# Performance work log

Measured on AMD Instinct MI355X. Metric: run time of the kernel, lower is better.

Reference implementation:

```python
import jax, jax.numpy as jnp
import numpy as np

B, D, K = 32, 400, 200
H = 8            # kernel_size (GRU hidden)
LAYERS = 4
OUT = 8


def setup_inputs() -> dict:
    key = jax.random.key(0)
    ks = jax.random.split(key, 16)
    x = jax.random.normal(ks[0], (B, D, K), dtype=jnp.float32)
    # variable-length zero padding along time per (b, k) sequence
    lengths = jax.random.randint(ks[1], (B, K), D // 2, D + 1)
    tmask = jnp.arange(D)[None, :, None] < lengths[:, None, :]   # (B, D, K)
    x = x * tmask
    s = 1.0 / np.sqrt(H)
    def u(k, shape):
        return jax.random.uniform(k, shape, jnp.float32, -s, s)
    return {
        "x": x,
        "w_ih0": u(ks[2], (2, 3 * H, 1)),
        "w_hh0": u(ks[3], (2, 3 * H, H)),
        "b_ih0": u(ks[4], (2, 3 * H)),
        "b_hh0": u(ks[5], (2, 3 * H)),
        "w_ih": u(ks[6], (LAYERS - 1, 2, 3 * H, 2 * H)),
        "w_hh": u(ks[7], (LAYERS - 1, 2, 3 * H, H)),
        "b_ih": u(ks[8], (LAYERS - 1, 2, 3 * H)),
        "b_hh": u(ks[9], (LAYERS - 1, 2, 3 * H)),
        "lin1_w": u(ks[10], (H, 2 * H)),
        "lin1_b": u(ks[11], (H,)),
        "lin2_w": u(ks[12], (OUT, H)),
        "lin2_b": u(ks[13], (OUT,)),
    }


def _gru_dir(x, mask, Wih, Whh, bih, bhh):
    # x: (N, T, in), mask: (N, T) bool -> (N, T, H); zero past each length
    gi = jnp.einsum('nti,gi->tng', x, Wih) + bih          # (T, N, 3H) input gates
    m = mask.T[:, :, None]                                 # (T, N, 1)
    h0 = jnp.zeros((x.shape[0], Whh.shape[1]), x.dtype)
    def step(h, inp):
        gi_t, m_t = inp
        gh = h @ Whh.T + bhh
        ir, iz, inn = jnp.split(gi_t, 3, axis=-1)          # PyTorch gate order r, z, n
        hr, hz, hn = jnp.split(gh, 3, axis=-1)
        r = jax.nn.sigmoid(ir + hr)
        z = jax.nn.sigmoid(iz + hz)
        n = jnp.tanh(inn + r * hn)
        h = jnp.where(m_t, (1.0 - z) * n + z * h, h)
        return h, jnp.where(m_t, h, 0.0)
    _, out = jax.lax.scan(step, h0, (gi, m))
    return out.transpose(1, 0, 2)


def _bidir_gru(x, mask, rev_idx, p):
    Wih, Whh, bih, bhh = p
    fwd = _gru_dir(x, mask, Wih[0], Whh[0], bih[0], bhh[0])
    # backward dir of a packed sequence: reverse within each valid region
    x_rev = jnp.take_along_axis(x, rev_idx[:, :, None], axis=1)
    bwd_rev = _gru_dir(x_rev, mask, Wih[1], Whh[1], bih[1], bhh[1])
    bwd = jnp.take_along_axis(bwd_rev, rev_idx[:, :, None], axis=1)
    bwd = jnp.where(mask[:, :, None], bwd, 0.0)
    return jnp.concatenate([fwd, bwd], axis=-1)


def _forward(x, w_ih0, w_hh0, b_ih0, b_hh0, w_ih, w_hh, b_ih, b_hh,
             lin1_w, lin1_b, lin2_w, lin2_b):
    b, d, k = x.shape
    seq = x.transpose(0, 2, 1).reshape(b * k, d, 1)         # (N, T, 1)
    vals = seq[:, :, 0]
    zm = vals == 0.0
    lengths = jnp.where(zm.any(axis=1), jnp.argmax(zm, axis=1), d)  # (N,)
    mask = jnp.arange(d)[None, :] < lengths[:, None]        # (N, T)
    rev_idx = jnp.clip(lengths[:, None] - 1 - jnp.arange(d)[None, :], 0, d - 1)
    h = _bidir_gru(seq, mask, rev_idx, (w_ih0, w_hh0, b_ih0, b_hh0))
    for l in range(w_ih.shape[0]):                          # layers 1..3
        h = _bidir_gru(h, mask, rev_idx, (w_ih[l], w_hh[l], b_ih[l], b_hh[l]))
    # last valid timestep per sequence (matches argmax-of-all-zero gather)
    last = jnp.take_along_axis(h, (lengths - 1)[:, None, None], axis=1)[:, 0, :]
    feat = last.reshape(b, k, -1)                           # (B, K, 2H)
    y = jax.nn.leaky_relu(feat @ lin1_w.T + lin1_b, negative_slope=0.2)
    return y @ lin2_w.T + lin2_b                            # (B, K, OUT)


def reference(x, w_ih0, w_hh0, b_ih0, b_hh0, w_ih, w_hh, b_ih, b_hh,
              lin1_w, lin1_b, lin2_w, lin2_b):
    return _forward(x, w_ih0, w_hh0, b_ih0, b_hh0, w_ih, w_hh, b_ih, b_hh,
                    lin1_w, lin1_b, lin2_w, lin2_b)
```

## Files before the change

kernel.cpp:

```cpp
#include <hip/hip_runtime.h>

#define BB 32
#define DD 400
#define KK 200
#define NN (BB*KK)
#define NBINS 512

typedef float f2 __attribute__((ext_vector_type(2)));
typedef _Float16 half_t;
typedef _Float16 f16x2 __attribute__((ext_vector_type(2)));

#if defined(__has_builtin)
#if __has_builtin(__builtin_amdgcn_fdot2)
#define HAVE_FDOT2 1
#endif
#endif

__device__ __forceinline__ float dot2(f16x2 w, f16x2 v, float acc) {
#ifdef HAVE_FDOT2
  return __builtin_amdgcn_fdot2(w, v, acc, false);
#else
  return fmaf((float)w.x, (float)v.x, fmaf((float)w.y, (float)v.y, acc));
#endif
}

__device__ __forceinline__ float fast_sigmoid(float x) {
  float e = __builtin_amdgcn_exp2f(-1.4426950408889634f * x);
  return __builtin_amdgcn_rcpf(1.0f + e);
}
__device__ __forceinline__ float fast_tanh(float x) {
  float e = __builtin_amdgcn_exp2f(-2.8853900817779268f * x);
  return 2.0f * __builtin_amdgcn_rcpf(1.0f + e) - 1.0f;
}

#define QPERM(v, P) __int_as_float(__builtin_amdgcn_mov_dpp(__float_as_int(v), (P)*0x55, 0xF, 0xF, true))
#define HMIRROR(v) __int_as_float(__builtin_amdgcn_mov_dpp(__float_as_int(v), 0x141, 0xF, 0xF, true))

__global__ __launch_bounds__(256) void transpose_x(const float* __restrict__ x,
                                                   float* __restrict__ xt) {
  __shared__ float tile[32][33];
  int b = blockIdx.x, t0 = blockIdx.y * 32, k0 = blockIdx.z * 32;
  int tx = threadIdx.x, ty = threadIdx.y;
#pragma unroll
  for (int i = 0; i < 32; i += 8) {
    int t = t0 + ty + i, k = k0 + tx;
    tile[ty + i][tx] = (t < DD && k < KK) ? x[((size_t)b * DD + t) * KK + k] : 0.0f;
  }
  __syncthreads();
#pragma unroll
  for (int i = 0; i < 32; i += 8) {
    int k = k0 + ty + i, t = t0 + tx;
    if (k < KK && t < DD) xt[((size_t)b * KK + k) * DD + t] = tile[tx][ty + i];
  }
}

__global__ __launch_bounds__(64) void compute_lengths(const float* __restrict__ xt,
                                                      int* __restrict__ lengths,
                                                      int* __restrict__ hist) {
  int n = blockIdx.x, lane = threadIdx.x;
  int m = DD;
  for (int t = lane; t < DD; t += 64) {
    if (xt[(size_t)n * DD + t] == 0.0f) { m = t; break; }
  }
#pragma unroll
  for (int off = 1; off < 64; off <<= 1) {
    int o = __shfl_xor(m, off, 64);
    m = (o < m) ? o : m;
  }
  if (lane == 0) {
    lengths[n] = m;
    atomicAdd(&hist[m], 1);
  }
}

__global__ __launch_bounds__(64) void scan_offsets(const int* __restrict__ hist,
                                                   int* __restrict__ offs) {
  int lane = threadIdx.x;
  int v[8], tot = 0;
#pragma unroll
  for (int i = 0; i < 8; ++i) { v[i] = tot; tot += hist[lane * 8 + i]; }
  int incl = tot;
#pragma unroll
  for (int off = 1; off < 64; off <<= 1) {
    int oth = __shfl_up(incl, off, 64);
    if (lane >= off) incl += oth;
  }
  int excl = incl - tot;
#pragma unroll
  for (int i = 0; i < 8; ++i) offs[lane * 8 + i] = excl + v[i];
}

__global__ __launch_bounds__(256) void scatter_sort(const int* __restrict__ lengths,
                                                    int* __restrict__ offs,
                                                    int* __restrict__ order,
                                                    int* __restrict__ len_sorted) {
  int n = blockIdx.x * 256 + threadIdx.x;
  if (n >= NN) return;
  int len = lengths[n];
  int pos = atomicAdd(&offs[len], 1);
  order[pos] = n;
  len_sorted[pos] = len;
}

template <int IN_DIM, bool IND_IN, bool WRITE_SEQ, bool FWD_ONLY>
__global__ __launch_bounds__(256) void gru_scan(
    const void* __restrict__ in, half_t* __restrict__ out, float* __restrict__ feat,
    const int* __restrict__ len_sorted, const int* __restrict__ order,
    const float* __restrict__ Wih, const float* __restrict__ Whh,
    const float* __restrict__ bih, const float* __restrict__ bhh, int nseq) {
  int p = (blockIdx.x * 256 + threadIdx.x) >> 6;
  int lane = threadIdx.x & 63;
  int G = FWD_ONLY ? nseq : nseq * 2;
  int W = (G + 7) >> 3;
  if (p >= W) return;
  int o = (p & 1) ? (W - 1 - (p >> 1)) : (p >> 1);
  int gidx = o * 8 + (lane >> 3);
  int li = lane & 7;
  if (gidx >= G) return;
  int sg  = FWD_ONLY ? gidx : (gidx >> 1);
  int dir = FWD_ONLY ? 0 : (gidx & 1);
  int len = len_sorted[sg];

  int qb = li & 4;
  f2 wAB[3][4];
  f16x2 wi2[3][8];
  float wi1[3];
  float bs[3], bh2;
#pragma unroll
  for (int gt = 0; gt < 3; ++gt) {
    int row = dir * 24 + gt * 8 + li;
    if constexpr (IN_DIM == 16) {
#pragma unroll
      for (int q = 0; q < 8; ++q) {
        f16x2 w;
        w.x = (half_t)Wih[row * 16 + 2 * q];
        w.y = (half_t)Wih[row * 16 + 2 * q + 1];
        wi2[gt][q] = w;
      }
    } else {
      wi1[gt] = Wih[row];
    }
#pragma unroll
    for (int P = 0; P < 4; ++P) {
      f2 w;
      w.x = Whh[row * 8 + qb + P];
      w.y = Whh[row * 8 + ((qb + P) ^ 7)];
      wAB[gt][P] = w;
    }
    bs[gt] = bih[row] + ((gt < 2) ? bhh[row] : 0.0f);
    if (gt == 2) bh2 = bhh[row];
  }

  int steps = len;
  float h = 0.0f;

  const float* px = nullptr;
  const half_t* pxh = nullptr;
  ptrdiff_t xstep;
  if constexpr (IN_DIM == 1) {
    const float* basep = (const float*)in + (IND_IN ? (size_t)order[sg] * DD : (size_t)sg * DD);
    px = basep + ((dir == 0) ? 0 : (len - 1));
    xstep = (dir == 0) ? 1 : -1;
  } else {
    const half_t* basep = (const half_t*)in + (size_t)sg * DD * 16;
    pxh = basep + (size_t)((dir == 0) ? 0 : (len - 1)) * 16;
    xstep = (dir == 0) ? 16 : -16;
  }

  half_t* pw = nullptr; ptrdiff_t wstep = 0;
  if constexpr (WRITE_SEQ) {
    pw = out + ((size_t)sg * DD + ((dir == 0) ? 0 : (len - 1))) * 16 + dir * 8 + li;
    wstep = (dir == 0) ? 16 : -16;
  }

  auto core = [&](float a0, float a1, float a2) {
    float hm = HMIRROR(h);
    float hq0 = QPERM(h, 0), hq1 = QPERM(h, 1), hq2 = QPERM(h, 2), hq3 = QPERM(h, 3);
    float hx0 = QPERM(hm, 0), hx1 = QPERM(hm, 1), hx2 = QPERM(hm, 2), hx3 = QPERM(hm, 3);
    f2 u0; u0.x = hq0; u0.y = hx0;
    f2 u1; u1.x = hq1; u1.y = hx1;
    f2 u2; u2.x = hq2; u2.y = hx2;
    f2 u3; u3.x = hq3; u3.y = hx3;

    f2 c0 = wAB[0][0] * u0; c0 += wAB[0][1] * u1; c0 += wAB[0][2] * u2; c0 += wAB[0][3] * u3;
    f2 c1 = wAB[1][0] * u0; c1 += wAB[1][1] * u1; c1 += wAB[1][2] * u2; c1 += wAB[1][3] * u3;
    f2 c2; c2.x = bh2; c2.y = 0.0f;
    c2 += wAB[2][0] * u0; c2 += wAB[2][1] * u1; c2 += wAB[2][2] * u2; c2 += wAB[2][3] * u3;

    float r = fast_sigmoid(a0 + c0.x + c0.y);
    float z = fast_sigmoid(a1 + c1.x + c1.y);
    float n = fast_tanh(a2 + r * (c2.x + c2.y));
    h = z * (h - n) + n;
    if constexpr (WRITE_SEQ) { *pw = (half_t)h; pw += wstep; }
  };

  if constexpr (IN_DIM == 1) {
    float s0_, s1_, s2_, s3_;
    auto ld = [&](float& S_) { S_ = *px; px += xstep; };
    auto st = [&](float& S_, bool pf) {
      float a0 = fmaf(wi1[0], S_, bs[0]);
      float a1 = fmaf(wi1[1], S_, bs[1]);
      float a2 = fmaf(wi1[2], S_, bs[2]);
      if (pf) ld(S_);
      core(a0, a1, a2);
    };
    ld(s0_); ld(s1_); ld(s2_); ld(s3_);
    int t = 0;
    for (; t + 4 <= steps; t += 4) {
      st(s0_, true); st(s1_, true); st(s2_, true); st(s3_, true);
    }
    int rem = steps - t;
    if (rem > 0) st(s0_, false);
    if (rem > 1) st(s1_, false);
    if (rem > 2) st(s2_, false);
  } else {
    uint4 b0_[2], b1_[2], b2_[2], b3_[2];
    auto ld = [&](uint4 (&B_)[2]) {
      const uint4* q4 = reinterpret_cast<const uint4*>(pxh);
      B_[0] = q4[0]; B_[1] = q4[1];
      pxh += xstep;
    };
    auto st = [&](uint4 (&B_)[2], bool pf) {
      float a0 = bs[0], a1 = bs[1], a2 = bs[2];
#pragma unroll
      for (int q = 0; q < 2; ++q) {
        f16x2 p0 = __builtin_bit_cast(f16x2, B_[q].x);
        f16x2 p1 = __builtin_bit_cast(f16x2, B_[q].y);
        f16x2 p2 = __builtin_bit_cast(f16x2, B_[q].z);
        f16x2 p3 = __builtin_bit_cast(f16x2, B_[q].w);
        a0 = dot2(wi2[0][4*q], p0, a0); a0 = dot2(wi2[0][4*q+1], p1, a0);
        a0 = dot2(wi2[0][4*q+2], p2, a0); a0 = dot2(wi2[0][4*q+3], p3, a0);
        a1 = dot2(wi2[1][4*q], p0, a1); a1 = dot2(wi2[1][4*q+1], p1, a1);
        a1 = dot2(wi2[1][4*q+2], p2, a1); a1 = dot2(wi2[1][4*q+3], p3, a1);
        a2 = dot2(wi2[2][4*q], p0, a2); a2 = dot2(wi2[2][4*q+1], p1, a2);
        a2 = dot2(wi2[2][4*q+2], p2, a2); a2 = dot2(wi2[2][4*q+3], p3, a2);
      }
      if (pf) ld(B_);
      core(a0, a1, a2);
    };
    ld(b0_); ld(b1_); ld(b2_); ld(b3_);
    int t = 0;
    for (; t + 4 <= steps; t += 4) {
      st(b0_, true); st(b1_, true); st(b2_, true); st(b3_, true);
    }
    int rem = steps - t;
    if (rem > 0) st(b0_, false);
    if (rem > 1) st(b1_, false);
    if (rem > 2) st(b2_, false);
  }

  if constexpr (!WRITE_SEQ) {
    feat[(size_t)order[sg] * 16 + dir * 8 + li] = h;
  }
}

__global__ __launch_bounds__(256) void bwd_last(
    const half_t* __restrict__ in, float* __restrict__ feat,
    const int* __restrict__ len_sorted, const int* __restrict__ order,
    const float* __restrict__ Wih, const float* __restrict__ bih,
    const float* __restrict__ bhh, int nseq) {
  int tid = blockIdx.x * blockDim.x + threadIdx.x;
  int sg = tid >> 3, li = tid & 7;
  if (sg >= nseq) return;
  int len = len_sorted[sg];
  const half_t* xp = in + ((size_t)sg * DD + (len - 1)) * 16;
  float xv[16];
#pragma unroll
  for (int j = 0; j < 16; ++j) xv[j] = (float)xp[j];
  float a[3], bh[3];
#pragma unroll
  for (int gt = 0; gt < 3; ++gt) {
    int row = 24 + gt * 8 + li;
    const float* wp = Wih + row * 16;
    float acc = bih[row];
#pragma unroll
    for (int j = 0; j < 16; ++j) acc = fmaf(wp[j], xv[j], acc);
    a[gt] = acc;
    bh[gt] = bhh[row];
  }
  float r = fast_sigmoid(a[0] + bh[0]);
  float z = fast_sigmoid(a[1] + bh[1]);
  float n = fast_tanh(a[2] + r * bh[2]);
  float h = (1.0f - z) * n;
  feat[(size_t)order[sg] * 16 + 8 + li] = h;
}

__global__ __launch_bounds__(256) void head_kernel(
    const float* __restrict__ feat, const float* __restrict__ w1,
    const float* __restrict__ b1, const float* __restrict__ w2,
    const float* __restrict__ b2, float* __restrict__ out) {
  int n = blockIdx.x * blockDim.x + threadIdx.x;
  if (n >= NN) return;
  float f[16];
  const float4* p = reinterpret_cast<const float4*>(feat + (size_t)n * 16);
#pragma unroll
  for (int q = 0; q < 4; ++q) {
    float4 v = p[q];
    f[4*q] = v.x; f[4*q+1] = v.y; f[4*q+2] = v.z; f[4*q+3] = v.w;
  }
  float y[8];
#pragma unroll
  for (int o = 0; o < 8; ++o) {
    float s = b1[o];
#pragma unroll
    for (int j = 0; j < 16; ++j) s += f[j] * w1[o * 16 + j];
    y[o] = (s > 0.0f) ? s : 0.2f * s;
  }
#pragma unroll
  for (int o2 = 0; o2 < 8; ++o2) {
    float s = b2[o2];
#pragma unroll
    for (int o = 0; o < 8; ++o) s += y[o] * w2[o2 * 8 + o];
    out[(size_t)n * 8 + o2] = s;
  }
}

extern "C" void kernel_launch(void* const* d_in, const int* in_sizes, int n_in,
                              void* d_out, int out_size, void* d_ws, size_t ws_size,
                              hipStream_t stream) {
  const float* x      = (const float*)d_in[0];
  const float* w_ih0  = (const float*)d_in[1];
  const float* w_hh0  = (const float*)d_in[2];
  const float* b_ih0  = (const float*)d_in[3];
  const float* b_hh0  = (const float*)d_in[4];
  const float* w_ih   = (const float*)d_in[5];
  const float* w_hh   = (const float*)d_in[6];
  const float* b_ih   = (const float*)d_in[7];
  const float* b_hh   = (const float*)d_in[8];
  const float* lin1_w = (const float*)d_in[9];
  const float* lin1_b = (const float*)d_in[10];
  const float* lin2_w = (const float*)d_in[11];
  const float* lin2_b = (const float*)d_in[12];
  float* out = (float*)d_out;

  char* ws = (char*)d_ws;
  size_t off = 0;
  auto alloc = [&](size_t bytes) -> void* {
    void* p = ws + off;
    off += (bytes + 255) & ~(size_t)255;
    return p;
  };
  alloc(1024);
  float* xt         = (float*)alloc((size_t)NN * DD * sizeof(float) + 1024);
  int*   lengths    = (int*)  alloc((size_t)NN * sizeof(int));
  int*   hist       = (int*)  alloc(NBINS * sizeof(int));
  int*   offs       = (int*)  alloc(NBINS * sizeof(int));
  int*   order      = (int*)  alloc((size_t)NN * sizeof(int));
  int*   len_sorted = (int*)  alloc((size_t)NN * sizeof(int));
  float* feat       = (float*)alloc((size_t)NN * 16 * sizeof(float));
  size_t base = off;
  size_t per_seq = (size_t)DD * 16 * sizeof(half_t) * 2 + 1024;
  int Nc = NN;
  if (base + (size_t)NN * per_seq + 8192 > ws_size) {
    size_t avail = (ws_size > base + 8192) ? (ws_size - base - 8192) : 0;
    size_t nc = avail / per_seq;
    if (nc < 1) nc = 1;
    if (nc > (size_t)NN) nc = NN;
    Nc = (int)nc;
  }
  alloc(1024);
  half_t* bufA = (half_t*)alloc((size_t)Nc * DD * 16 * sizeof(half_t) + 1024);
  half_t* bufB = (half_t*)alloc((size_t)Nc * DD * 16 * sizeof(half_t) + 1024);

  hipMemsetAsync(hist, 0, NBINS * sizeof(int), stream);
  dim3 gT(BB, (DD + 31) / 32, (KK + 31) / 32), bT(32, 8, 1);
  hipLaunchKernelGGL(transpose_x, gT, bT, 0, stream, x, xt);
  hipLaunchKernelGGL(compute_lengths, dim3(NN), dim3(64), 0, stream, xt, lengths, hist);
  hipLaunchKernelGGL(scan_offsets, dim3(1), dim3(64), 0, stream, hist, offs);
  hipLaunchKernelGGL(scatter_sort, dim3((NN + 255) / 256), dim3(256), 0, stream,
                     lengths, offs, order, len_sorted);

  for (int s0 = 0; s0 < NN; s0 += Nc) {
    int ns = (NN - s0 < Nc) ? (NN - s0) : Nc;
    int W2 = (ns * 2 + 7) / 8;
    int W1 = (ns + 7) / 8;
    int blk2 = (W2 + 3) / 4;
    int blk1f = (W1 + 3) / 4;
    int blk1 = (ns * 8 + 255) / 256;
    gru_scan<1, true, true, false><<<blk2, 256, 0, stream>>>(
        (const void*)xt, bufA, nullptr, len_sorted + s0, order + s0,
        w_ih0, w_hh0, b_ih0, b_hh0, ns);
    gru_scan<16, false, true, false><<<blk2, 256, 0, stream>>>(
        (const void*)bufA, bufB, nullptr, len_sorted + s0, order + s0,
        w_ih + 0 * 2 * 24 * 16, w_hh + 0 * 2 * 24 * 8,
        b_ih + 0 * 2 * 24, b_hh + 0 * 2 * 24, ns);
    gru_scan<16, false, true, false><<<blk2, 256, 0, stream>>>(
        (const void*)bufB, bufA, nullptr, len_sorted + s0, order + s0,
        w_ih + 1 * 2 * 24 * 16, w_hh + 1 * 2 * 24 * 8,
        b_ih + 1 * 2 * 24, b_hh + 1 * 2 * 24, ns);
    gru_scan<16, false, false, true><<<blk1f, 256, 0, stream>>>(
        (const void*)bufA, nullptr, feat, len_sorted + s0, order + s0,
        w_ih + 2 * 2 * 24 * 16, w_hh + 2 * 2 * 24 * 8,
        b_ih + 2 * 2 * 24, b_hh + 2 * 2 * 24, ns);
    hipLaunchKernelGGL(bwd_last, dim3(blk1), dim3(256), 0, stream,
                       bufA, feat, len_sorted + s0, order + s0,
                       w_ih + 2 * 2 * 24 * 16, b_ih + 2 * 2 * 24, b_hh + 2 * 2 * 24, ns);
  }
  hipLaunchKernelGGL(head_kernel, dim3((NN + 255) / 256), dim3(256), 0, stream,
                     feat, lin1_w, lin1_b, lin2_w, lin2_b, out);
}
```

Baseline: 462.2 us.

## Launch one wave per block and balance octet-to-SIMD assignment by length

The GRU scan kernels now launch one 64-thread wave per block instead of four waves per 256-thread block, and a new mapping assigns length-sorted sequence octets to waves. The aim is for the first NSIMD waves to take the longest work while the rest pair up so that total work per SIMD slot evens out. The recurrent matvec accumulation is also split into two independent partial sums per gate to shorten the dependency chain on the serial critical path. Risks are extra block-scheduling overhead and that the balancing assumes a fixed slot count (1024) matching the hardware.

```diff
diff --git a/kernel.cpp b/kernel.cpp
--- a/kernel.cpp
+++ b/kernel.cpp
@@ -5,6 +5,7 @@
 #define KK 200
 #define NN (BB*KK)
 #define NBINS 512
+#define NSIMD 1024
 
 typedef float f2 __attribute__((ext_vector_type(2)));
 typedef _Float16 half_t;
@@ -102,18 +103,26 @@
   len_sorted[pos] = len;
 }
 
+__device__ __forceinline__ int octet_of_wave(int p, int W) {
+  int E = W - NSIMD;
+  if (E <= 0) return W - 1 - p;
+  if (p >= NSIMD) return p - NSIMD;
+  if (p >= E) return W - 1 - (p - E);
+  return (W - 1 - NSIMD + E) - p;
+}
+
 template <int IN_DIM, bool IND_IN, bool WRITE_SEQ, bool FWD_ONLY>
-__global__ __launch_bounds__(256) void gru_scan(
+__global__ __launch_bounds__(64) void gru_scan(
     const void* __restrict__ in, half_t* __restrict__ out, float* __restrict__ feat,
     const int* __restrict__ len_sorted, const int* __restrict__ order,
     const float* __restrict__ Wih, const float* __restrict__ Whh,
     const float* __restrict__ bih, const float* __restrict__ bhh, int nseq) {
-  int p = (blockIdx.x * 256 + threadIdx.x) >> 6;
+  int p = blockIdx.x;
   int lane = threadIdx.x & 63;
   int G = FWD_ONLY ? nseq : nseq * 2;
   int W = (G + 7) >> 3;
   if (p >= W) return;
-  int o = (p & 1) ? (W - 1 - (p >> 1)) : (p >> 1);
+  int o = octet_of_wave(p, W);
   int gidx = o * 8 + (lane >> 3);
   int li = lane & 7;
   if (gidx >= G) return;
@@ -182,14 +191,19 @@
     f2 u2; u2.x = hq2; u2.y = hx2;
     f2 u3; u3.x = hq3; u3.y = hx3;
 
-    f2 c0 = wAB[0][0] * u0; c0 += wAB[0][1] * u1; c0 += wAB[0][2] * u2; c0 += wAB[0][3] * u3;
-    f2 c1 = wAB[1][0] * u0; c1 += wAB[1][1] * u1; c1 += wAB[1][2] * u2; c1 += wAB[1][3] * u3;
-    f2 c2; c2.x = bh2; c2.y = 0.0f;
-    c2 += wAB[2][0] * u0; c2 += wAB[2][1] * u1; c2 += wAB[2][2] * u2; c2 += wAB[2][3] * u3;
+    f2 c0a = wAB[0][0] * u0; c0a += wAB[0][1] * u1;
+    f2 c0b = wAB[0][2] * u2; c0b += wAB[0][3] * u3;
+    f2 c0 = c0a + c0b;
+    f2 c1a = wAB[1][0] * u0; c1a += wAB[1][1] * u1;
+    f2 c1b = wAB[1][2] * u2; c1b += wAB[1][3] * u3;
+    f2 c1 = c1a + c1b;
+    f2 c2a = wAB[2][0] * u0; c2a += wAB[2][1] * u1;
+    f2 c2b = wAB[2][2] * u2; c2b += wAB[2][3] * u3;
+    f2 c2 = c2a + c2b;
 
     float r = fast_sigmoid(a0 + c0.x + c0.y);
     float z = fast_sigmoid(a1 + c1.x + c1.y);
-    float n = fast_tanh(a2 + r * (c2.x + c2.y));
+    float n = fast_tanh(a2 + r * (bh2 + c2.x + c2.y));
     h = z * (h - n) + n;
     if constexpr (WRITE_SEQ) { *pw = (half_t)h; pw += wstep; }
   };
@@ -374,21 +388,19 @@
     int ns = (NN - s0 < Nc) ? (NN - s0) : Nc;
     int W2 = (ns * 2 + 7) / 8;
     int W1 = (ns + 7) / 8;
-    int blk2 = (W2 + 3) / 4;
-    int blk1f = (W1 + 3) / 4;
     int blk1 = (ns * 8 + 255) / 256;
-    gru_scan<1, true, true, false><<<blk2, 256, 0, stream>>>(
+    gru_scan<1, true, true, false><<<W2, 64, 0, stream>>>(
         (const void*)xt, bufA, nullptr, len_sorted + s0, order + s0,
         w_ih0, w_hh0, b_ih0, b_hh0, ns);
-    gru_scan<16, false, true, false><<<blk2, 256, 0, stream>>>(
+    gru_scan<16, false, true, false><<<W2, 64, 0, stream>>>(
         (const void*)bufA, bufB, nullptr, len_sorted + s0, order + s0,
         w_ih + 0 * 2 * 24 * 16, w_hh + 0 * 2 * 24 * 8,
         b_ih + 0 * 2 * 24, b_hh + 0 * 2 * 24, ns);
-    gru_scan<16, false, true, false><<<blk2, 256, 0, stream>>>(
+    gru_scan<16, false, true, false><<<W2, 64, 0, stream>>>(
         (const void*)bufB, bufA, nullptr, len_sorted + s0, order + s0,
         w_ih + 1 * 2 * 24 * 16, w_hh + 1 * 2 * 24 * 8,
         b_ih + 1 * 2 * 24, b_hh + 1 * 2 * 24, ns);
-    gru_scan<16, false, false, true><<<blk1f, 256, 0, stream>>>(
+    gru_scan<16, false, false, true><<<W1, 64, 0, stream>>>(
         (const void*)bufA, nullptr, feat, len_sorted + s0, order + s0,
         w_ih + 2 * 2 * 24 * 16, w_hh + 2 * 2 * 24 * 8,
         b_ih + 2 * 2 * 24, b_hh + 2 * 2 * 24, ns);
```

Result: faster. 414.8 us (-10.3%).
